# Kernel tuning notes

Hardware: AMD Instinct MI355X
Metric: run time of the kernel (lower is better)

## Reference

```python
import jax, jax.numpy as jnp
import numpy as np

EPS = 1e-5
NUM_GROUPS = 32
NUM_HEADS = 4


def setup_inputs() -> dict:
    key = jax.random.key(0)
    ks = jax.random.split(key, 3)
    B, C, H, W = 4, 256, 64, 64
    x = jax.random.normal(ks[0], (B, C, H, W), dtype=jnp.float32)
    gn_w = jnp.ones((C,), jnp.float32)
    gn_b = jnp.zeros((C,), jnp.float32)
    qkv_w = jax.random.normal(ks[1], (3 * C, C), dtype=jnp.float32) * (C ** -0.5)
    qkv_b = jnp.zeros((3 * C,), jnp.float32)
    proj_w = jax.random.normal(ks[2], (C, C), dtype=jnp.float32) * (C ** -0.5)
    proj_b = jnp.zeros((C,), jnp.float32)
    return {"x": x, "gn_w": gn_w, "gn_b": gn_b, "qkv_w": qkv_w,
            "qkv_b": qkv_b, "proj_w": proj_w, "proj_b": proj_b}


def _group_norm(x, w, b):
    B, C, H, W = x.shape
    xg = x.reshape(B, NUM_GROUPS, C // NUM_GROUPS, H, W)
    mean = xg.mean(axis=(2, 3, 4), keepdims=True)
    var = xg.var(axis=(2, 3, 4), keepdims=True)
    xn = ((xg - mean) * jax.lax.rsqrt(var + EPS)).reshape(B, C, H, W)
    return xn * w[None, :, None, None] + b[None, :, None, None]


def reference(x, gn_w, gn_b, qkv_w, qkv_b, proj_w, proj_b):
    B, C, H, W = x.shape
    nh = NUM_HEADS
    d = C // nh
    L = H * W
    h = _group_norm(x, gn_w, gn_b)
    # 1x1 conv == channel matmul
    qkv = jnp.einsum('oc,bchw->bohw', qkv_w, h) + qkv_b[None, :, None, None]
    q, k, v = jnp.split(qkv, 3, axis=1)
    # (B, C, H, W) -> (B, nh, L, d)
    def to_heads(t):
        return t.reshape(B, nh, d, L).transpose(0, 1, 3, 2)
    q, k, v = to_heads(q), to_heads(k), to_heads(v)
    scale = d ** -0.5
    attn = jax.nn.softmax(jnp.einsum('bhqd,bhkd->bhqk', q, k) * scale, axis=-1)
    o = jnp.einsum('bhqk,bhkd->bhqd', attn, v)          # (B, nh, L, d)
    o = o.transpose(0, 1, 3, 2).reshape(B, C, H, W)
    o = jnp.einsum('oc,bchw->bohw', proj_w, o) + proj_b[None, :, None, None]
    return x + o
```

## Files before the change

### kernel.cpp

```cpp
#include <hip/hip_runtime.h>

#define B_   4
#define C_   256
#define L_   4096
#define NH_  4
#define D_   64
#define G_   32
#define CPG_ 8

typedef __bf16 bf16x8 __attribute__((ext_vector_type(8)));
typedef float  f32x4  __attribute__((ext_vector_type(4)));

__device__ __forceinline__ ushort f2bf(float f) {
  union { float f; unsigned u; } c; c.f = f;
  unsigned u = c.u;
  return (ushort)((u + 0x7fffu + ((u >> 16) & 1u)) >> 16);
}
__device__ __forceinline__ float bf2f(ushort h) {
  union { unsigned u; float f; } c; c.u = ((unsigned)h) << 16; return c.f;
}
__device__ __forceinline__ unsigned fbits(float f) {
  union { float f; unsigned u; } c; c.f = f; return c.u;
}
__device__ __forceinline__ float fastexp2(float x) {
#if __has_builtin(__builtin_amdgcn_exp2f)
  return __builtin_amdgcn_exp2f(x);
#else
  return exp2f(x);
#endif
}

__global__ __launch_bounds__(256) void cvt_kernel(const float* __restrict__ wq,
                                                  const float* __restrict__ wp,
                                                  ushort* __restrict__ oq,
                                                  ushort* __restrict__ op,
                                                  float* __restrict__ stats) {
  int t = blockIdx.x * 256 + threadIdx.x;
  if (blockIdx.x == 0) stats[threadIdx.x] = 0.f;
  const int NQ4 = (768 * 256) / 4;
  float4 v;
  if (t < NQ4) {
    v = ((const float4*)wq)[t];
    ((ushort4*)oq)[t] = make_ushort4(f2bf(v.x), f2bf(v.y), f2bf(v.z), f2bf(v.w));
  } else {
    int i = t - NQ4;
    v = ((const float4*)wp)[i];
    ((ushort4*)op)[i] = make_ushort4(f2bf(v.x), f2bf(v.y), f2bf(v.z), f2bf(v.w));
  }
}

__global__ __launch_bounds__(256) void gn_stats(const float* __restrict__ x,
                                                float* __restrict__ stats) {
  int bg = blockIdx.x >> 3, chunk = blockIdx.x & 7;
  int b = bg >> 5, g = bg & 31;
  const float* xg = x + ((size_t)b * C_ + g * CPG_) * L_ + chunk * 512;
  int tid = threadIdx.x;

  float s = 0.f, ss = 0.f;
  for (int c = 0; c < CPG_; ++c) {
    float2 v = ((const float2*)(xg + (size_t)c * L_))[tid];
    s  += v.x + v.y;
    ss += v.x * v.x + v.y * v.y;
  }
  for (int off = 32; off; off >>= 1) { s += __shfl_xor(s, off); ss += __shfl_xor(ss, off); }
  __shared__ float red[8];
  int w = tid >> 6;
  if ((tid & 63) == 0) { red[w] = s; red[4 + w] = ss; }
  __syncthreads();
  if (tid == 0) {
    atomicAdd(&stats[bg * 2],     red[0] + red[1] + red[2] + red[3]);
    atomicAdd(&stats[bg * 2 + 1], red[4] + red[5] + red[6] + red[7]);
  }
}

__global__ __launch_bounds__(256) void gn_apply(const float* __restrict__ x,
                                                const float* __restrict__ gw,
                                                const float* __restrict__ gb,
                                                const float* __restrict__ stats,
                                                ushort* __restrict__ hT) {
  int bg = blockIdx.x >> 3, chunk = blockIdx.x & 7;
  int b = bg >> 5, g = bg & 31;
  const float* xg = x + ((size_t)b * C_ + g * CPG_) * L_;
  int tid = threadIdx.x;

  const float inv_n = 1.0f / (CPG_ * L_);
  float mean = stats[bg * 2] * inv_n;
  float var  = stats[bg * 2 + 1] * inv_n - mean * mean;
  float rstd = rsqrtf(var + 1e-5f);

  float wv[CPG_], bv[CPG_];
  for (int c = 0; c < CPG_; ++c) { wv[c] = gw[g * CPG_ + c]; bv[c] = gb[g * CPG_ + c]; }

  for (int li = 0; li < 2; ++li) {
    int l = chunk * 512 + li * 256 + tid;
    union { ushort s[8]; uint4 u; } o;
    for (int c = 0; c < CPG_; ++c) {
      float v = xg[(size_t)c * L_ + l];
      o.s[c] = f2bf((v - mean) * rstd * wv[c] + bv[c]);
    }
    *(uint4*)(hT + ((size_t)b * L_ + l) * C_ + g * CPG_) = o.u;
  }
}

__global__ __launch_bounds__(256) void qkv_kernel(const ushort* __restrict__ hT,
                                                  const ushort* __restrict__ w,
                                                  const float* __restrict__ bias,
                                                  ushort* __restrict__ q,
                                                  ushort* __restrict__ k,
                                                  ushort* __restrict__ v) {
  int wid  = blockIdx.x * 4 + (threadIdx.x >> 6);
  int lane = threadIdx.x & 63;
  int quad = lane >> 4, col = lane & 15;
  int ot   = wid % 12;
  int rest = wid / 12;
  int lt   = rest & 127;
  int b    = rest >> 7;
  int o0 = ot * 64, l0 = lt * 32;

  const ushort* abase = w  + (size_t)(o0 + col) * C_ + quad * 8;
  const ushort* bbase = hT + ((size_t)b * L_ + l0 + col) * C_ + quad * 8;

  f32x4 acc[4][2];
  for (int i = 0; i < 4; ++i) for (int j = 0; j < 2; ++j)
    acc[i][j] = (f32x4){0.f, 0.f, 0.f, 0.f};

  for (int k0 = 0; k0 < C_; k0 += 32) {
    bf16x8 a[4], bb[2];
#pragma unroll
    for (int i = 0; i < 4; ++i) a[i]  = *(const bf16x8*)(abase + (size_t)(i * 16) * C_ + k0);
#pragma unroll
    for (int j = 0; j < 2; ++j) bb[j] = *(const bf16x8*)(bbase + (size_t)(j * 16) * C_ + k0);
#pragma unroll
    for (int i = 0; i < 4; ++i)
#pragma unroll
      for (int j = 0; j < 2; ++j)
        acc[i][j] = __builtin_amdgcn_mfma_f32_16x16x32_bf16(a[i], bb[j], acc[i][j], 0, 0, 0);
  }

  int third = o0 >> 8;
  int hh    = (o0 & 255) >> 6;
  float scale = (third == 0) ? 0.180336880111120f : 1.0f;
#pragma unroll
  for (int i = 0; i < 4; ++i) {
    int oo = o0 + i * 16 + quad * 4;
    int dd = i * 16 + quad * 4;
#pragma unroll
    for (int j = 0; j < 2; ++j) {
      int l = l0 + j * 16 + col;
      ushort pk[4];
      for (int r = 0; r < 4; ++r) pk[r] = f2bf((acc[i][j][r] + bias[oo + r]) * scale);
      if (third < 2) {
        ushort* dst = (third ? k : q) + (((size_t)(b * NH_ + hh) * L_ + l) * D_ + dd);
        *(ushort4*)dst = make_ushort4(pk[0], pk[1], pk[2], pk[3]);
      } else {
        for (int r = 0; r < 4; ++r)
          v[((size_t)(b * NH_ + hh) * D_ + dd + r) * L_ + l] = pk[r];
      }
    }
  }
}

__global__ __launch_bounds__(256) void attn_kernel(const ushort* __restrict__ q,
                                                   const ushort* __restrict__ k,
                                                   const ushort* __restrict__ v,
                                                   ushort* __restrict__ p0,
                                                   ushort* __restrict__ p1,
                                                   float* __restrict__ psumbuf) {
  __shared__ __align__(16) ushort k_lds[64][72];
  __shared__ __align__(16) ushort v_lds[64][72];

  int tid   = threadIdx.x;
  int w     = tid >> 6, lane = tid & 63;
  int quad  = lane >> 4, col = lane & 15;
  int split = blockIdx.x >> 9;
  int bh    = (blockIdx.x >> 5) & 15;
  int qblk  = blockIdx.x & 31;

  const ushort* qp = q + (size_t)bh * L_ * D_;
  const ushort* kp = k + (size_t)bh * L_ * D_;
  const ushort* vp = v + (size_t)bh * D_ * L_;

  int qrow0 = qblk * 128 + w * 32;
  bf16x8 bq[2][2];
#pragma unroll
  for (int f = 0; f < 2; ++f)
#pragma unroll
    for (int c = 0; c < 2; ++c)
      bq[f][c] = *(const bf16x8*)(qp + (size_t)(qrow0 + f * 16 + col) * D_ + c * 32 + quad * 8);

  f32x4 oacc[2][4];
#pragma unroll
  for (int f = 0; f < 2; ++f)
    for (int t = 0; t < 4; ++t) oacc[f][t] = (f32x4){0.f, 0.f, 0.f, 0.f};
  float psum[2] = {0.f, 0.f};

  int vrow = tid >> 2, vchunk = tid & 3;
  int kt0 = split * (L_ / 2);

  for (int kt = kt0; kt < kt0 + L_ / 2; kt += 64) {
    __syncthreads();
    {
      const uint4* ksrc = (const uint4*)(kp + (size_t)kt * D_);
      uint4 k0 = ksrc[tid];
      uint4 k1 = ksrc[tid + 256];
      *(uint4*)&k_lds[tid >> 3][(tid & 7) * 8] = k0;
      *(uint4*)&k_lds[32 + (tid >> 3)][(tid & 7) * 8] = k1;
      const uint4* vsrc = (const uint4*)(vp + (size_t)vrow * L_ + kt);
      uint4 v0 = vsrc[vchunk * 2];
      uint4 v1 = vsrc[vchunk * 2 + 1];
      *(uint4*)&v_lds[vrow][vchunk * 16] = v0;
      *(uint4*)&v_lds[vrow][vchunk * 16 + 8] = v1;
    }
    __syncthreads();

#pragma unroll
    for (int h = 0; h < 2; ++h) {
      f32x4 s0[2], s1[2];
#pragma unroll
      for (int f = 0; f < 2; ++f) { s0[f] = (f32x4){0.f,0.f,0.f,0.f}; s1[f] = (f32x4){0.f,0.f,0.f,0.f}; }
#pragma unroll
      for (int c = 0; c < 2; ++c) {
        bf16x8 a0 = *(const bf16x8*)&k_lds[h * 32 + col][c * 32 + quad * 8];
        bf16x8 a1 = *(const bf16x8*)&k_lds[h * 32 + 16 + col][c * 32 + quad * 8];
#pragma unroll
        for (int f = 0; f < 2; ++f) {
          s0[f] = __builtin_amdgcn_mfma_f32_16x16x32_bf16(a0, bq[f][c], s0[f], 0, 0, 0);
          s1[f] = __builtin_amdgcn_mfma_f32_16x16x32_bf16(a1, bq[f][c], s1[f], 0, 0, 0);
        }
      }

      bf16x8 pb[2];
#pragma unroll
      for (int f = 0; f < 2; ++f) {
        float pe0[4], pe1[4];
#pragma unroll
        for (int r = 0; r < 4; ++r) {
          pe0[r] = fastexp2(s0[f][r]);
          pe1[r] = fastexp2(s1[f][r]);
          psum[f] += pe0[r] + pe1[r];
        }
        union { unsigned u[4]; bf16x8 v8; } pc;
        pc.u[0] = __builtin_amdgcn_perm(fbits(pe0[1]), fbits(pe0[0]), 0x07060302u);
        pc.u[1] = __builtin_amdgcn_perm(fbits(pe0[3]), fbits(pe0[2]), 0x07060302u);
        pc.u[2] = __builtin_amdgcn_perm(fbits(pe1[1]), fbits(pe1[0]), 0x07060302u);
        pc.u[3] = __builtin_amdgcn_perm(fbits(pe1[3]), fbits(pe1[2]), 0x07060302u);
        pb[f] = pc.v8;
      }

#pragma unroll
      for (int t = 0; t < 4; ++t) {
        union { uint2 u2[2]; bf16x8 v8; } vc;
        vc.u2[0] = *(const uint2*)&v_lds[t * 16 + col][h * 32 + quad * 4];
        vc.u2[1] = *(const uint2*)&v_lds[t * 16 + col][h * 32 + 16 + quad * 4];
        bf16x8 av = vc.v8;
#pragma unroll
        for (int f = 0; f < 2; ++f)
          oacc[f][t] = __builtin_amdgcn_mfma_f32_16x16x32_bf16(av, pb[f], oacc[f][t], 0, 0, 0);
      }
    }
  }

  ushort* po = split ? p1 : p0;
#pragma unroll
  for (int f = 0; f < 2; ++f) {
    psum[f] += __shfl_xor(psum[f], 16);
    psum[f] += __shfl_xor(psum[f], 32);
    for (int t = 0; t < 4; ++t) {
      ushort ok[4];
      for (int r = 0; r < 4; ++r) ok[r] = f2bf(oacc[f][t][r]);
      ushort* dst = po + ((size_t)bh * L_ + qrow0 + f * 16 + col) * D_ + t * 16 + quad * 4;
      *(ushort4*)dst = make_ushort4(ok[0], ok[1], ok[2], ok[3]);
    }
    if (quad == 0)
      psumbuf[split * (16 * L_) + bh * L_ + qrow0 + f * 16 + col] = psum[f];
  }
}

__global__ __launch_bounds__(256) void comb_kernel(ushort* __restrict__ p0,
                                                   const ushort* __restrict__ p1,
                                                   const float* __restrict__ ps) {
  int idx = blockIdx.x * 256 + threadIdx.x;
  int row = idx >> 4;
  float inv = 1.0f / (ps[row] + ps[16 * L_ + row]);
  ushort4 a = ((const ushort4*)p0)[idx];
  ushort4 b = ((const ushort4*)p1)[idx];
  ((ushort4*)p0)[idx] = make_ushort4(
      f2bf((bf2f(a.x) + bf2f(b.x)) * inv),
      f2bf((bf2f(a.y) + bf2f(b.y)) * inv),
      f2bf((bf2f(a.z) + bf2f(b.z)) * inv),
      f2bf((bf2f(a.w) + bf2f(b.w)) * inv));
}

__global__ __launch_bounds__(256) void proj_kernel(const ushort* __restrict__ oin,
                                                   const ushort* __restrict__ pw,
                                                   const float* __restrict__ pb,
                                                   const float* __restrict__ x,
                                                   float* __restrict__ out) {
  int wid  = blockIdx.x * 4 + (threadIdx.x >> 6);
  int lane = threadIdx.x & 63;
  int quad = lane >> 4, col = lane & 15;
  int oct  = wid & 7;
  int rest = wid >> 3;
  int lt   = rest & 127;
  int b    = rest >> 7;
  int l0 = lt * 32, oc0 = oct * 32;

  f32x4 acc[2][2];
  for (int i = 0; i < 2; ++i) for (int j = 0; j < 2; ++j)
    acc[i][j] = (f32x4){0.f, 0.f, 0.f, 0.f};

  for (int k0 = 0; k0 < C_; k0 += 32) {
    int hh = k0 >> 6, dk = k0 & 63;
    bf16x8 a[2], bb[2];
#pragma unroll
    for (int i = 0; i < 2; ++i)
      a[i] = *(const bf16x8*)(oin + ((size_t)(b * NH_ + hh) * L_ + l0 + i * 16 + col) * D_ + dk + quad * 8);
#pragma unroll
    for (int j = 0; j < 2; ++j)
      bb[j] = *(const bf16x8*)(pw + (size_t)(oc0 + j * 16 + col) * C_ + k0 + quad * 8);
#pragma unroll
    for (int i = 0; i < 2; ++i)
#pragma unroll
      for (int j = 0; j < 2; ++j)
        acc[i][j] = __builtin_amdgcn_mfma_f32_16x16x32_bf16(a[i], bb[j], acc[i][j], 0, 0, 0);
  }

#pragma unroll
  for (int j = 0; j < 2; ++j) {
    int oc = oc0 + j * 16 + col;
    float bias = pb[oc];
#pragma unroll
    for (int i = 0; i < 2; ++i) {
      int l = l0 + i * 16 + quad * 4;
      size_t off = ((size_t)b * C_ + oc) * L_ + l;
      float4 xv = *(const float4*)(x + off);
      float4 ov = make_float4(acc[i][j][0] + bias + xv.x,
                              acc[i][j][1] + bias + xv.y,
                              acc[i][j][2] + bias + xv.z,
                              acc[i][j][3] + bias + xv.w);
      *(float4*)(out + off) = ov;
    }
  }
}

extern "C" void kernel_launch(void* const* d_in, const int* in_sizes, int n_in,
                              void* d_out, int out_size, void* d_ws, size_t ws_size,
                              hipStream_t stream) {
  const float* x      = (const float*)d_in[0];
  const float* gn_w   = (const float*)d_in[1];
  const float* gn_b   = (const float*)d_in[2];
  const float* qkv_w  = (const float*)d_in[3];
  const float* qkv_b  = (const float*)d_in[4];
  const float* proj_w = (const float*)d_in[5];
  const float* proj_b = (const float*)d_in[6];
  float* out = (float*)d_out;

  const size_t TEN = (size_t)B_ * C_ * L_;
  ushort* ws  = (ushort*)d_ws;
  ushort* q   = ws;
  ushort* k   = ws + TEN;
  ushort* v   = ws + 2 * TEN;
  ushort* oat = ws + 3 * TEN;
  ushort* wq  = ws + 4 * TEN;
  ushort* wp  = wq + 768 * 256;
  float*  stats = (float*)(wp + 256 * 256);
  ushort* hT  = (ushort*)d_out;
  ushort* p1  = (ushort*)d_out + TEN;
  float*  psb = (float*)d_out;

  cvt_kernel <<<256,       256, 0, stream>>>(qkv_w, proj_w, wq, wp, stats);
  gn_stats   <<<1024,      256, 0, stream>>>(x, stats);
  gn_apply   <<<1024,      256, 0, stream>>>(x, gn_w, gn_b, stats, hT);
  qkv_kernel <<<6144 / 4,  256, 0, stream>>>(hT, wq, qkv_b, q, k, v);
  attn_kernel<<<1024,      256, 0, stream>>>(q, k, v, oat, p1, psb);
  comb_kernel<<<4096,      256, 0, stream>>>(oat, p1, psb);
  proj_kernel<<<4096 / 4,  256, 0, stream>>>(oat, wp, proj_b, x, out);
}
```

Before: 236.3 us.

## Split attention keys three ways and compute row sums with MFMA

The attention kernel now splits the key range across three blocks instead of two, using 22/21/21 tiles, which raises the grid to 1536 blocks to fill the device better. Row-sum accumulation moves from scalar adds plus shuffles to an MFMA against a ones vector. Partial sums are combined with atomicAdd into a buffer that a new zero kernel clears first. The combine kernel sums three partial outputs. This adds an extra launch, atomics and more partial-output traffic, and reuses the wq workspace region for the sums after the QKV kernel has run.

```diff
diff --git a/kernel.cpp b/kernel.cpp
--- a/kernel.cpp
+++ b/kernel.cpp
@@ -160,12 +160,17 @@
   }
 }
 
+__global__ __launch_bounds__(256) void zer_kernel(float* __restrict__ psb) {
+  psb[blockIdx.x * 256 + threadIdx.x] = 0.f;
+}
+
 __global__ __launch_bounds__(256) void attn_kernel(const ushort* __restrict__ q,
                                                    const ushort* __restrict__ k,
                                                    const ushort* __restrict__ v,
                                                    ushort* __restrict__ p0,
                                                    ushort* __restrict__ p1,
-                                                   float* __restrict__ psumbuf) {
+                                                   ushort* __restrict__ p2,
+                                                   float* __restrict__ psb) {
   __shared__ __align__(16) ushort k_lds[64][72];
   __shared__ __align__(16) ushort v_lds[64][72];
 
@@ -188,16 +193,22 @@
     for (int c = 0; c < 2; ++c)
       bq[f][c] = *(const bf16x8*)(qp + (size_t)(qrow0 + f * 16 + col) * D_ + c * 32 + quad * 8);
 
-  f32x4 oacc[2][4];
-#pragma unroll
-  for (int f = 0; f < 2; ++f)
+  f32x4 oacc[2][4], psacc[2];
+#pragma unroll
+  for (int f = 0; f < 2; ++f) {
     for (int t = 0; t < 4; ++t) oacc[f][t] = (f32x4){0.f, 0.f, 0.f, 0.f};
-  float psum[2] = {0.f, 0.f};
+    psacc[f] = (f32x4){0.f, 0.f, 0.f, 0.f};
+  }
+
+  union { unsigned u[4]; bf16x8 v8; } onesu;
+  onesu.u[0] = onesu.u[1] = onesu.u[2] = onesu.u[3] = 0x3F803F80u;
+  const bf16x8 ones = onesu.v8;
 
   int vrow = tid >> 2, vchunk = tid & 3;
-  int kt0 = split * (L_ / 2);
-
-  for (int kt = kt0; kt < kt0 + L_ / 2; kt += 64) {
+  int t0 = (split == 0) ? 0 : (1 + split * 21);
+  int t1 = 22 + split * 21;
+
+  for (int kt = t0 * 64; kt < t1 * 64; kt += 64) {
     __syncthreads();
     {
       const uint4* ksrc = (const uint4*)(kp + (size_t)kt * D_);
@@ -237,7 +248,6 @@
         for (int r = 0; r < 4; ++r) {
           pe0[r] = fastexp2(s0[f][r]);
           pe1[r] = fastexp2(s1[f][r]);
-          psum[f] += pe0[r] + pe1[r];
         }
         union { unsigned u[4]; bf16x8 v8; } pc;
         pc.u[0] = __builtin_amdgcn_perm(fbits(pe0[1]), fbits(pe0[0]), 0x07060302u);
@@ -245,6 +255,7 @@
         pc.u[2] = __builtin_amdgcn_perm(fbits(pe1[1]), fbits(pe1[0]), 0x07060302u);
         pc.u[3] = __builtin_amdgcn_perm(fbits(pe1[3]), fbits(pe1[2]), 0x07060302u);
         pb[f] = pc.v8;
+        psacc[f] = __builtin_amdgcn_mfma_f32_16x16x32_bf16(ones, pb[f], psacc[f], 0, 0, 0);
       }
 
 #pragma unroll
@@ -260,11 +271,9 @@
     }
   }
 
-  ushort* po = split ? p1 : p0;
+  ushort* po = (split == 0) ? p0 : (split == 1) ? p1 : p2;
 #pragma unroll
   for (int f = 0; f < 2; ++f) {
-    psum[f] += __shfl_xor(psum[f], 16);
-    psum[f] += __shfl_xor(psum[f], 32);
     for (int t = 0; t < 4; ++t) {
       ushort ok[4];
       for (int r = 0; r < 4; ++r) ok[r] = f2bf(oacc[f][t][r]);
@@ -272,23 +281,25 @@
       *(ushort4*)dst = make_ushort4(ok[0], ok[1], ok[2], ok[3]);
     }
     if (quad == 0)
-      psumbuf[split * (16 * L_) + bh * L_ + qrow0 + f * 16 + col] = psum[f];
+      atomicAdd(&psb[bh * L_ + qrow0 + f * 16 + col], psacc[f][0]);
   }
 }
 
 __global__ __launch_bounds__(256) void comb_kernel(ushort* __restrict__ p0,
                                                    const ushort* __restrict__ p1,
-                                                   const float* __restrict__ ps) {
+                                                   const ushort* __restrict__ p2,
+                                                   const float* __restrict__ psb) {
   int idx = blockIdx.x * 256 + threadIdx.x;
   int row = idx >> 4;
-  float inv = 1.0f / (ps[row] + ps[16 * L_ + row]);
+  float inv = 1.0f / psb[row];
   ushort4 a = ((const ushort4*)p0)[idx];
   ushort4 b = ((const ushort4*)p1)[idx];
+  ushort4 c = ((const ushort4*)p2)[idx];
   ((ushort4*)p0)[idx] = make_ushort4(
-      f2bf((bf2f(a.x) + bf2f(b.x)) * inv),
-      f2bf((bf2f(a.y) + bf2f(b.y)) * inv),
-      f2bf((bf2f(a.z) + bf2f(b.z)) * inv),
-      f2bf((bf2f(a.w) + bf2f(b.w)) * inv));
+      f2bf((bf2f(a.x) + bf2f(b.x) + bf2f(c.x)) * inv),
+      f2bf((bf2f(a.y) + bf2f(b.y) + bf2f(c.y)) * inv),
+      f2bf((bf2f(a.z) + bf2f(b.z) + bf2f(c.z)) * inv),
+      f2bf((bf2f(a.w) + bf2f(b.w) + bf2f(c.w)) * inv));
 }
 
 __global__ __launch_bounds__(256) void proj_kernel(const ushort* __restrict__ oin,
@@ -360,19 +371,21 @@
   ushort* q   = ws;
   ushort* k   = ws + TEN;
   ushort* v   = ws + 2 * TEN;
-  ushort* oat = ws + 3 * TEN;
+  ushort* p0  = ws + 3 * TEN;
   ushort* wq  = ws + 4 * TEN;
   ushort* wp  = wq + 768 * 256;
   float*  stats = (float*)(wp + 256 * 256);
+  float*  psb = (float*)wq;
   ushort* hT  = (ushort*)d_out;
-  ushort* p1  = (ushort*)d_out + TEN;
-  float*  psb = (float*)d_out;
+  ushort* p1  = (ushort*)d_out;
+  ushort* p2  = (ushort*)d_out + TEN;
 
   cvt_kernel <<<256,       256, 0, stream>>>(qkv_w, proj_w, wq, wp, stats);
   gn_stats   <<<1024,      256, 0, stream>>>(x, stats);
   gn_apply   <<<1024,      256, 0, stream>>>(x, gn_w, gn_b, stats, hT);
   qkv_kernel <<<6144 / 4,  256, 0, stream>>>(hT, wq, qkv_b, q, k, v);
-  attn_kernel<<<1024,      256, 0, stream>>>(q, k, v, oat, p1, psb);
-  comb_kernel<<<4096,      256, 0, stream>>>(oat, p1, psb);
-  proj_kernel<<<4096 / 4,  256, 0, stream>>>(oat, wp, proj_b, x, out);
-}
+  zer_kernel <<<256,       256, 0, stream>>>(psb);
+  attn_kernel<<<1536,      256, 0, stream>>>(q, k, v, p0, p1, p2, psb);
+  comb_kernel<<<4096,      256, 0, stream>>>(p0, p1, p2, psb);
+  proj_kernel<<<4096 / 4,  256, 0, stream>>>(p0, wp, proj_b, x, out);
+}
```

New measurement: 241.1 us. 1.02x slower.
